# Kernel optimization log

Hardware: AMD Instinct MI355X
Metric: run time of the kernel (lower is better)

Reference implementation:

```python
import jax, jax.numpy as jnp
import numpy as np

VOCAB = 1_000_000
BATCH = 8192
SLOTS = 26
VEC = 128
NNZ = BATCH * SLOTS  # max_nnz=1 -> one value per (sample, slot) CSR row


def setup_inputs() -> dict:
    key = jax.random.key(0)
    k_tab, k_val = jax.random.split(key)
    # Learned embedding table (HugeCTR-internal parameter)
    table = jax.random.normal(k_tab, (VOCAB, VEC), dtype=jnp.float32) * 0.01
    # CSR: with max_nnz=1, each row holds exactly one index
    row_offsets = jnp.arange(NNZ + 1, dtype=jnp.int64)
    value_tensors = jax.random.randint(k_val, (NNZ,), 0, VOCAB, dtype=jnp.int64)
    nnz_array = NNZ
    output_shape = jnp.zeros((3,), dtype=jnp.int64)  # placeholder; static dims used below
    return {
        "table": table,
        "row_offsets": row_offsets,
        "value_tensors": value_tensors,
        "nnz_array": nnz_array,
        "output_shape": output_shape,
    }


def reference(table, row_offsets, value_tensors, nnz_array, output_shape):
    # Sparse embedding lookup + per-slot 'sum' combine over CSR rows.
    n_rows = BATCH * SLOTS
    total = value_tensors.shape[0]
    # segment id of value i = (# offsets <= i) - 1
    seg = jnp.searchsorted(row_offsets, jnp.arange(total), side="right") - 1
    emb = table[value_tensors]  # [total, VEC] irregular gather
    combined = jax.ops.segment_sum(emb, seg, num_segments=n_rows)  # sum combiner
    return combined.reshape(BATCH, SLOTS, VEC)
```

## Files before the change

### kernel.cpp

```cpp
#include <hip/hip_runtime.h>


#define ROW_F4 32

__global__ __launch_bounds__(256) void plugin_embedding_gather(
    const float4* __restrict__ table,
    const int*    __restrict__ row_offsets,
    const int*    __restrict__ vals,
    float4*       __restrict__ out,
    int n_rows)
{
    int t   = blockIdx.x * blockDim.x + threadIdx.x;
    int row = t >> 5;
    int col = t & 31;
    if (row >= n_rows) return;

    int start = row_offsets[row];
    int end   = row_offsets[row + 1];

    float4 acc = make_float4(0.f, 0.f, 0.f, 0.f);
    for (int j = start; j < end; ++j) {
        int idx = vals[j];
        float4 v = table[(size_t)idx * ROW_F4 + col];
        acc.x += v.x; acc.y += v.y; acc.z += v.z; acc.w += v.w;
    }
    out[(size_t)row * ROW_F4 + col] = acc;
}

extern "C" void kernel_launch(void* const* d_in, const int* in_sizes, int n_in,
                              void* d_out, int out_size, void* d_ws, size_t ws_size,
                              hipStream_t stream) {
    const float4* table       = (const float4*)d_in[0];
    const int*    row_offsets = (const int*)d_in[1];
    const int*    vals        = (const int*)d_in[2];
    float4*       out         = (float4*)d_out;

    int n_rows = out_size / 128;

    long long total_threads = (long long)n_rows * ROW_F4;
    int block = 256;
    int grid  = (int)((total_threads + block - 1) / block);

    plugin_embedding_gather<<<grid, block, 0, stream>>>(
        table, row_offsets, vals, out, n_rows);
}
```

Baseline: 607.9 us.

## Process four rows per half-wave with batched index and table loads

Each 64-lane wave now covers eight CSR rows, with each half-wave handling four of them. All row offsets, then all indices, then all first table rows are loaded up front so several independent gathers are in flight per thread. Remaining nonzeros are accumulated afterwards, and outputs are written with nontemporal stores so the streamed result does not pollute cache. The grid shrinks by four times, so there are fewer threads to hide latency, traded against more memory-level parallelism per thread.

```diff
diff --git a/kernel.cpp b/kernel.cpp
--- a/kernel.cpp
+++ b/kernel.cpp
@@ -2,42 +2,82 @@
 
 
 #define ROW_F4 32
+#define U 4
+
+typedef float f32x4 __attribute__((ext_vector_type(4)));
 
 __global__ __launch_bounds__(256) void plugin_embedding_gather(
-    const float4* __restrict__ table,
-    const int*    __restrict__ row_offsets,
-    const int*    __restrict__ vals,
-    float4*       __restrict__ out,
+    const f32x4* __restrict__ table,
+    const int*   __restrict__ row_offsets,
+    const int*   __restrict__ vals,
+    f32x4*       __restrict__ out,
     int n_rows)
 {
-    int t   = blockIdx.x * blockDim.x + threadIdx.x;
-    int row = t >> 5;
-    int col = t & 31;
-    if (row >= n_rows) return;
+    int t    = blockIdx.x * blockDim.x + threadIdx.x;
+    int lane = t & 63;
+    int col  = lane & 31;
+    int half = lane >> 5;
+    long long wid = t >> 6;
+    int base = (int)(wid * (2 * U)) + half;
 
-    int start = row_offsets[row];
-    int end   = row_offsets[row + 1];
+    int row[U], s[U], e[U], idx[U];
+    bool live[U];
 
-    float4 acc = make_float4(0.f, 0.f, 0.f, 0.f);
-    for (int j = start; j < end; ++j) {
-        int idx = vals[j];
-        float4 v = table[(size_t)idx * ROW_F4 + col];
-        acc.x += v.x; acc.y += v.y; acc.z += v.z; acc.w += v.w;
+    #pragma unroll
+    for (int u = 0; u < U; ++u) {
+        row[u]  = base + 2 * u;
+        live[u] = (row[u] < n_rows);
+        if (live[u]) {
+            s[u] = row_offsets[row[u]];
+            e[u] = row_offsets[row[u] + 1];
+        } else {
+            s[u] = 0; e[u] = 0;
+        }
     }
-    out[(size_t)row * ROW_F4 + col] = acc;
+
+    #pragma unroll
+    for (int u = 0; u < U; ++u)
+        idx[u] = (s[u] < e[u]) ? vals[s[u]] : -1;
+
+    f32x4 acc[U];
+    #pragma unroll
+    for (int u = 0; u < U; ++u) {
+        if (idx[u] >= 0) {
+            acc[u] = table[(size_t)idx[u] * ROW_F4 + col];
+        } else {
+            acc[u] = (f32x4)(0.f, 0.f, 0.f, 0.f);
+        }
+    }
+
+    #pragma unroll
+    for (int u = 0; u < U; ++u) {
+        for (int j = s[u] + 1; j < e[u]; ++j) {
+            int id2 = vals[j];
+            f32x4 v = table[(size_t)id2 * ROW_F4 + col];
+            acc[u] += v;
+        }
+    }
+
+    #pragma unroll
+    for (int u = 0; u < U; ++u) {
+        if (live[u]) {
+            __builtin_nontemporal_store(acc[u], &out[(size_t)row[u] * ROW_F4 + col]);
+        }
+    }
 }
 
 extern "C" void kernel_launch(void* const* d_in, const int* in_sizes, int n_in,
                               void* d_out, int out_size, void* d_ws, size_t ws_size,
                               hipStream_t stream) {
-    const float4* table       = (const float4*)d_in[0];
-    const int*    row_offsets = (const int*)d_in[1];
-    const int*    vals        = (const int*)d_in[2];
-    float4*       out         = (float4*)d_out;
+    const f32x4* table       = (const f32x4*)d_in[0];
+    const int*   row_offsets = (const int*)d_in[1];
+    const int*   vals        = (const int*)d_in[2];
+    f32x4*       out         = (f32x4*)d_out;
 
     int n_rows = out_size / 128;
 
-    long long total_threads = (long long)n_rows * ROW_F4;
+    long long waves         = ((long long)n_rows + 2 * U - 1) / (2 * U);
+    long long total_threads = waves * 64;
     int block = 256;
     int grid  = (int)((total_threads + block - 1) / block);
 
```

Result: no change. 609.5 us (+0.3%).
